# Kernel tuning notes

Measured on AMD Instinct MI355X. Metric: run time of the kernel, lower is better.

Reference implementation:

```python
import jax, jax.numpy as jnp
import numpy as np

EMBED_DIM = 1024
NUM_HEADS = 16
PROJ_DIM = EMBED_DIM // NUM_HEADS


def setup_inputs() -> dict:
    key = jax.random.key(0)
    ks = jax.random.split(key, 9)
    s = 1.0 / np.sqrt(EMBED_DIM)
    inp = {
        "inputs": jax.random.normal(ks[0], (4, 2048, EMBED_DIM), dtype=jnp.float32),
        "Wq": jax.random.normal(ks[1], (EMBED_DIM, EMBED_DIM), dtype=jnp.float32) * s,
        "bq": jnp.zeros((EMBED_DIM,), jnp.float32),
        "Wk": jax.random.normal(ks[2], (EMBED_DIM, EMBED_DIM), dtype=jnp.float32) * s,
        "bk": jnp.zeros((EMBED_DIM,), jnp.float32),
        "Wv": jax.random.normal(ks[3], (EMBED_DIM, EMBED_DIM), dtype=jnp.float32) * s,
        "bv": jnp.zeros((EMBED_DIM,), jnp.float32),
        "Wo": jax.random.normal(ks[4], (EMBED_DIM, EMBED_DIM), dtype=jnp.float32) * s,
        "bo": jnp.zeros((EMBED_DIM,), jnp.float32),
    }
    return inp


def _split_heads(x):
    # [B, S, E] -> [B, H, S, D]
    b, s, _ = x.shape
    return x.reshape(b, s, NUM_HEADS, PROJ_DIM).transpose(0, 2, 1, 3)


def reference(inputs, Wq, bq, Wk, bk, Wv, bv, Wo, bo):
    q = _split_heads(inputs @ Wq + bq)
    k = _split_heads(inputs @ Wk + bk)
    v = _split_heads(inputs @ Wv + bv)
    scale = 1.0 / jnp.sqrt(jnp.asarray(PROJ_DIM, inputs.dtype))
    scores = jnp.einsum("bhqd,bhkd->bhqk", q, k) * scale  # [B,H,S,S]
    weights = jax.nn.softmax(scores, axis=-1)
    attn = jnp.einsum("bhqk,bhkd->bhqd", weights, v)
    b, h, s, d = attn.shape
    concat = attn.transpose(0, 2, 1, 3).reshape(b, s, h * d)
    return concat @ Wo + bo
```

## Files before the change

kernel.cpp:

```cpp
#include <hip/hip_runtime.h>
#include <math.h>

#define EMB 1024
#define SEQ 2048
#define BATCH 4
#define NH 16
#define HD 64
#define MTOT (BATCH * SEQ)

typedef _Float16 half_t;
typedef _Float16 half8 __attribute__((ext_vector_type(8)));
typedef __fp16 fp16x2 __attribute__((ext_vector_type(2)));
typedef float floatx4 __attribute__((ext_vector_type(4)));
typedef float floatx16 __attribute__((ext_vector_type(16)));

#if __has_builtin(__builtin_amdgcn_exp2f)
#define EXP2(x) __builtin_amdgcn_exp2f(x)
#else
#define EXP2(x) exp2f(x)
#endif

#define QSCALE 0.18033688f

__device__ __forceinline__ unsigned pkh(float a, float b) {
  union { fp16x2 h; unsigned u; } c;
  c.h = __builtin_amdgcn_cvt_pkrtz(a, b);
  return c.u;
}

__global__ __launch_bounds__(256) void conv_all(const float* __restrict__ x,
                                                half_t* __restrict__ xh,
                                                const float* __restrict__ W0,
                                                const float* __restrict__ W1,
                                                const float* __restrict__ W2,
                                                const float* __restrict__ W3,
                                                half_t* __restrict__ wt) {
  __shared__ float T[64][68];
  const int bid = blockIdx.x;
  const int t = threadIdx.x;
  if (bid < 4096) {
    int i = bid * 256 + t;
    float4 a = ((const float4*)x)[i * 2];
    float4 b = ((const float4*)x)[i * 2 + 1];
    float v[8] = {a.x, a.y, a.z, a.w, b.x, b.y, b.z, b.w};
    half8 o;
#pragma unroll
    for (int j = 0; j < 8; ++j) o[j] = (half_t)v[j];
    *(half8*)(xh + (size_t)i * 8) = o;
    return;
  }
  const int b2 = bid - 4096;
  const int z = b2 >> 8, rem = b2 & 255;
  const int k0 = (rem >> 4) * 64, n0 = (rem & 15) * 64;
  const float* W = (z == 0) ? W0 : (z == 1) ? W1 : (z == 2) ? W2 : W3;
  half_t* wto = wt + (size_t)z * 1048576;
#pragma unroll
  for (int i = 0; i < 4; ++i) {
    int idx = t + i * 256;
    int row = idx >> 4, c4 = (idx & 15) << 2;
    *(float4*)(&T[row][c4]) = *(const float4*)(W + (size_t)(k0 + row) * EMB + n0 + c4);
  }
  __syncthreads();
#pragma unroll
  for (int cc = 0; cc < 2; ++cc) {
    int c = t + cc * 256;
    int n = c >> 3, g = c & 7;
    half8 hh;
#pragma unroll
    for (int j = 0; j < 8; ++j) hh[j] = (half_t)T[g * 8 + j][n];
    *(half8*)(wto + (size_t)(n0 + n) * EMB + k0 + g * 8) = hh;
  }
}

__global__ __launch_bounds__(256) void gemm_qkv(const half_t* __restrict__ A,
                                                const half_t* __restrict__ WT,
                                                const float* __restrict__ bq,
                                                const float* __restrict__ bk,
                                                const float* __restrict__ bvv,
                                                half_t* __restrict__ Qh,
                                                half_t* __restrict__ Kh,
                                                half_t* __restrict__ Vt) {
  __shared__ half_t lds[17408];
  half_t* As = lds;
  half_t* Bs = lds + 5120;

  const int mat = blockIdx.x;
  const half_t* B = WT + (size_t)mat * 1048576;
  const float* bias = (mat == 0) ? bq : (mat == 1) ? bk : bvv;
  const float scale = (mat == 0) ? QSCALE : 1.0f;
  half_t* outh = (mat == 0) ? Qh : (mat == 1) ? Kh : Vt;

  const int t = threadIdx.x;
  const int l = t & 63, w = t >> 6;
  const int wm = w >> 1, wn = w & 1;
  const int lr = l & 15, lg = l >> 4;
  const int row0 = blockIdx.y * 128, col0 = blockIdx.z * 128;
  const int sr = t >> 2, sg = t & 3;

  floatx4 acc[4][4];
#pragma unroll
  for (int i = 0; i < 4; ++i)
#pragma unroll
    for (int j = 0; j < 4; ++j) acc[i][j] = (floatx4){0.f, 0.f, 0.f, 0.f};

  for (int kb = 0; kb < EMB; kb += 32) {
    half8 a0 = *(const half8*)(A + (size_t)(row0 + sr) * EMB + kb + sg * 8);
    half8 a1 = *(const half8*)(A + (size_t)(row0 + sr + 64) * EMB + kb + sg * 8);
    half8 b0 = *(const half8*)(B + (size_t)(col0 + sr) * EMB + kb + sg * 8);
    half8 b1 = *(const half8*)(B + (size_t)(col0 + sr + 64) * EMB + kb + sg * 8);
    __syncthreads();
    *(half8*)(As + sr * 40 + sg * 8) = a0;
    *(half8*)(As + (sr + 64) * 40 + sg * 8) = a1;
    *(half8*)(Bs + sr * 40 + sg * 8) = b0;
    *(half8*)(Bs + (sr + 64) * 40 + sg * 8) = b1;
    __syncthreads();

    half8 fa[4];
#pragma unroll
    for (int mf = 0; mf < 4; ++mf)
      fa[mf] = *(const half8*)(As + (wm * 64 + mf * 16 + lr) * 40 + lg * 8);
#pragma unroll
    for (int nf = 0; nf < 4; ++nf) {
      half8 fb = *(const half8*)(Bs + (wn * 64 + nf * 16 + lr) * 40 + lg * 8);
#pragma unroll
      for (int mf = 0; mf < 4; ++mf)
        acc[mf][nf] = __builtin_amdgcn_mfma_f32_16x16x32_f16(fa[mf], fb, acc[mf][nf], 0, 0, 0);
    }
  }

  float bv[4];
#pragma unroll
  for (int nf = 0; nf < 4; ++nf) bv[nf] = bias[col0 + wn * 64 + nf * 16 + lr];

  if (mat < 2) {
#pragma unroll
    for (int mf = 0; mf < 4; ++mf)
#pragma unroll
      for (int nf = 0; nf < 4; ++nf)
#pragma unroll
        for (int r = 0; r < 4; ++r) {
          int row = row0 + wm * 64 + mf * 16 + lg * 4 + r;
          int col = col0 + wn * 64 + nf * 16 + lr;
          int bb = row >> 11, ss = row & (SEQ - 1);
          int hh = col >> 6, dd = col & (HD - 1);
          float f = (acc[mf][nf][r] + bv[nf]) * scale;
          outh[((size_t)(bb * NH + hh) * SEQ + ss) * HD + dd] = (half_t)f;
        }
  } else {
    half_t* T = lds;
    const int bb = row0 >> 11, s0 = row0 & (SEQ - 1);
    __syncthreads();
#pragma unroll
    for (int mf = 0; mf < 4; ++mf)
#pragma unroll
      for (int nf = 0; nf < 4; ++nf)
#pragma unroll
        for (int r = 0; r < 4; ++r) {
          float f = acc[mf][nf][r] + bv[nf];
          T[(wm * 64 + mf * 16 + lg * 4 + r) * 136 + wn * 64 + nf * 16 + lr] = (half_t)f;
        }
    __syncthreads();
#pragma unroll
    for (int i = 0; i < 8; ++i) {
      int idx = t + i * 256;
      int n = idx >> 4, mg = idx & 15;
      int col = col0 + n;
      int hh = col >> 6, dd = col & (HD - 1);
      half8 pk;
#pragma unroll
      for (int j = 0; j < 8; ++j) pk[j] = T[(mg * 8 + j) * 136 + n];
      *(half8*)(outh + ((size_t)(bb * NH + hh) * HD + dd) * SEQ + s0 + mg * 8) = pk;
    }
  }
}

__global__ __launch_bounds__(256) void gemmo(const half_t* __restrict__ A,
                                             const half_t* __restrict__ B,
                                             const float* __restrict__ bias,
                                             float* __restrict__ outf) {
  __shared__ half_t lds[10240];
  half_t* As = lds;
  half_t* Bs = lds + 5120;

  const int t = threadIdx.x;
  const int l = t & 63, w = t >> 6;
  const int wm = w >> 1, wn = w & 1;
  const int lr = l & 15, lg = l >> 4;
  const int row0 = blockIdx.x * 128, col0 = blockIdx.y * 128;
  const int sr = t >> 2, sg = t & 3;

  floatx4 acc[4][4];
#pragma unroll
  for (int i = 0; i < 4; ++i)
#pragma unroll
    for (int j = 0; j < 4; ++j) acc[i][j] = (floatx4){0.f, 0.f, 0.f, 0.f};

  for (int kb = 0; kb < EMB; kb += 32) {
    half8 a0 = *(const half8*)(A + (size_t)(row0 + sr) * EMB + kb + sg * 8);
    half8 a1 = *(const half8*)(A + (size_t)(row0 + sr + 64) * EMB + kb + sg * 8);
    half8 b0 = *(const half8*)(B + (size_t)(col0 + sr) * EMB + kb + sg * 8);
    half8 b1 = *(const half8*)(B + (size_t)(col0 + sr + 64) * EMB + kb + sg * 8);
    __syncthreads();
    *(half8*)(As + sr * 40 + sg * 8) = a0;
    *(half8*)(As + (sr + 64) * 40 + sg * 8) = a1;
    *(half8*)(Bs + sr * 40 + sg * 8) = b0;
    *(half8*)(Bs + (sr + 64) * 40 + sg * 8) = b1;
    __syncthreads();

    half8 fa[4];
#pragma unroll
    for (int mf = 0; mf < 4; ++mf)
      fa[mf] = *(const half8*)(As + (wm * 64 + mf * 16 + lr) * 40 + lg * 8);
#pragma unroll
    for (int nf = 0; nf < 4; ++nf) {
      half8 fb = *(const half8*)(Bs + (wn * 64 + nf * 16 + lr) * 40 + lg * 8);
#pragma unroll
      for (int mf = 0; mf < 4; ++mf)
        acc[mf][nf] = __builtin_amdgcn_mfma_f32_16x16x32_f16(fa[mf], fb, acc[mf][nf], 0, 0, 0);
    }
  }

  float bv[4];
#pragma unroll
  for (int nf = 0; nf < 4; ++nf) bv[nf] = bias[col0 + wn * 64 + nf * 16 + lr];
#pragma unroll
  for (int mf = 0; mf < 4; ++mf)
#pragma unroll
    for (int nf = 0; nf < 4; ++nf)
#pragma unroll
      for (int r = 0; r < 4; ++r) {
        int row = row0 + wm * 64 + mf * 16 + lg * 4 + r;
        int col = col0 + wn * 64 + nf * 16 + lr;
        outf[(size_t)row * EMB + col] = acc[mf][nf][r] + bv[nf];
      }
}

__global__ __launch_bounds__(512) void attnh(const half_t* __restrict__ Q,
                                             const half_t* __restrict__ K,
                                             const half_t* __restrict__ Vt,
                                             half_t* __restrict__ att) {
  __shared__ half_t lds[2 * 4608];
  half_t* Ks = lds;
  half_t* Vs = lds + 4608;

  const int t = threadIdx.x, l = t & 63, wq = t >> 6;
  const int lq = l & 31, hi = l >> 5;
  const int hi8 = hi * 8, hi4 = hi * 4;
  const int q0 = blockIdx.x * 256;
  const int bh = blockIdx.y;
  const size_t kbase = (size_t)bh * SEQ * HD;
  const size_t vbase = (size_t)bh * HD * SEQ;
  const int srow = t >> 3, sg = t & 7;

  half8 qf[4];
  const int qrow = q0 + wq * 32 + lq;
#pragma unroll
  for (int s = 0; s < 4; ++s)
    qf[s] = *(const half8*)(Q + kbase + (size_t)qrow * HD + s * 16 + hi8);

  floatx16 o0, o1;
#pragma unroll
  for (int r = 0; r < 16; ++r) { o0[r] = 0.f; o1[r] = 0.f; }
  float l_s = 0.f;

  half8 kh_r = *(const half8*)(K + kbase + (size_t)srow * HD + sg * 8);
  half8 vh_r = *(const half8*)(Vt + vbase + (size_t)srow * SEQ + sg * 8);

  for (int kv = 0; kv < SEQ; kv += 64) {
    __syncthreads();
    *(half8*)(Ks + srow * 72 + sg * 8) = kh_r;
    *(half8*)(Vs + srow * 72 + sg * 8) = vh_r;
    __syncthreads();

    {
      int nk = (kv + 64) & (SEQ - 1);
      kh_r = *(const half8*)(K + kbase + (size_t)(nk + srow) * HD + sg * 8);
      vh_r = *(const half8*)(Vt + vbase + (size_t)srow * SEQ + nk + sg * 8);
    }

    floatx16 s0v, s1v;
#pragma unroll
    for (int r = 0; r < 16; ++r) { s0v[r] = 0.f; s1v[r] = 0.f; }
#pragma unroll
    for (int s = 0; s < 4; ++s) {
      const int off = s * 16 + hi8;
      half8 kf0 = *(const half8*)(Ks + lq * 72 + off);
      half8 kf1 = *(const half8*)(Ks + (32 + lq) * 72 + off);
      s0v = __builtin_amdgcn_mfma_f32_32x32x16_f16(kf0, qf[s], s0v, 0, 0, 0);
      s1v = __builtin_amdgcn_mfma_f32_32x32x16_f16(kf1, qf[s], s1v, 0, 0, 0);
    }

    float rsum = 0.f;
#pragma unroll
    for (int r = 0; r < 16; ++r) { s0v[r] = EXP2(s0v[r]); rsum += s0v[r]; }
#pragma unroll
    for (int r = 0; r < 16; ++r) { s1v[r] = EXP2(s1v[r]); rsum += s1v[r]; }
    rsum += __shfl_xor(rsum, 32);
    l_s += rsum;

#define PV_STEP(SC, RH, S)                                                    \
  {                                                                           \
    unsigned u0 = pkh(SC[(RH) * 8 + 0], SC[(RH) * 8 + 1]);                    \
    unsigned u1 = pkh(SC[(RH) * 8 + 2], SC[(RH) * 8 + 3]);                    \
    unsigned u2 = pkh(SC[(RH) * 8 + 4], SC[(RH) * 8 + 5]);                    \
    unsigned u3 = pkh(SC[(RH) * 8 + 6], SC[(RH) * 8 + 7]);                    \
    asm volatile("v_permlane32_swap_b32 %0, %1" : "+v"(u0), "+v"(u2));        \
    asm volatile("v_permlane32_swap_b32 %0, %1" : "+v"(u1), "+v"(u3));        \
    int4 pi = make_int4((int)u0, (int)u1, (int)u2, (int)u3);                  \
    half8 pa = *(half8*)&pi;                                                  \
    half8 vb0 = *(const half8*)(Vs + lq * 72 + (S) * 16 + hi8);               \
    half8 vb1 = *(const half8*)(Vs + (32 + lq) * 72 + (S) * 16 + hi8);        \
    o0 = __builtin_amdgcn_mfma_f32_32x32x16_f16(pa, vb0, o0, 0, 0, 0);        \
    o1 = __builtin_amdgcn_mfma_f32_32x32x16_f16(pa, vb1, o1, 0, 0, 0);        \
  }
    PV_STEP(s0v, 0, 0)
    PV_STEP(s0v, 1, 1)
    PV_STEP(s1v, 0, 2)
    PV_STEP(s1v, 1, 3)
#undef PV_STEP
  }

  float inv = 1.f / l_s;
  float il[16];
#pragma unroll
  for (int r = 0; r < 16; ++r)
    il[r] = __shfl(inv, ((r & 3) + 8 * (r >> 2)) + hi4);
  const int bb2 = bh >> 4, hh2 = bh & 15;
#pragma unroll
  for (int dblk = 0; dblk < 2; ++dblk)
#pragma unroll
    for (int r = 0; r < 16; ++r) {
      float f = (dblk ? o1[r] : o0[r]) * il[r];
      int qg = q0 + wq * 32 + ((r & 3) + 8 * (r >> 2)) + hi4;
      size_t off = ((size_t)bb2 * SEQ + qg) * EMB + hh2 * HD + dblk * 32 + lq;
      att[off] = (half_t)f;
    }
}

extern "C" void kernel_launch(void* const* d_in, const int* in_sizes, int n_in,
                              void* d_out, int out_size, void* d_ws, size_t ws_size,
                              hipStream_t stream) {
  const float* X  = (const float*)d_in[0];
  const float* Wq = (const float*)d_in[1];
  const float* bq = (const float*)d_in[2];
  const float* Wk = (const float*)d_in[3];
  const float* bk = (const float*)d_in[4];
  const float* Wv = (const float*)d_in[5];
  const float* bv = (const float*)d_in[6];
  const float* Wo = (const float*)d_in[7];
  const float* bo = (const float*)d_in[8];
  float* out = (float*)d_out;

  char* wsb = (char*)d_ws;
  const size_t MB = 1024 * 1024;
  half_t* Xh = (half_t*)(wsb);
  half_t* WT = (half_t*)(wsb + 17 * MB);
  half_t* Qh = (half_t*)(wsb + 26 * MB);
  half_t* Kh = (half_t*)(wsb + 43 * MB);
  half_t* Vt = (half_t*)d_out;
  half_t* att = Xh;

  half_t* WTq = WT;
  half_t* WTo = WT + 3145728;

  conv_all<<<dim3(5120), 256, 0, stream>>>(X, Xh, Wq, Wk, Wv, Wo, WT);

  gemm_qkv<<<dim3(3, MTOT / 128, EMB / 128), 256, 0, stream>>>(
      Xh, WTq, bq, bk, bv, Qh, Kh, Vt);

  attnh<<<dim3(SEQ / 256, BATCH * NH), 512, 0, stream>>>(Qh, Kh, Vt, att);

  gemmo<<<dim3(MTOT / 128, EMB / 128), 256, 0, stream>>>(att, WTo, bo, out);
}
```

Baseline: 223.8 us.

## Load GEMM tiles directly into LDS with XOR-swizzled unpadded layout

Both projection GEMMs now use global_load_lds (16-byte direct global-to-LDS loads) instead of loading into registers and storing to shared memory. The padded 40-half row stride becomes an unpadded 32-half stride with an XOR swizzle on the 8-half chunk index to avoid bank conflicts on fragment reads. The V transpose staging buffer stride also changes from 136 to 137. This removes the register round-trip and shrinks LDS use, but keeps single buffering with two barriers per k-step, so load latency is still not overlapped.

Result: faster. 196.9 us (-12.0%).

```diff
diff --git a/kernel.cpp b/kernel.cpp
--- a/kernel.cpp
+++ b/kernel.cpp
@@ -21,6 +21,11 @@
 #endif
 
 #define QSCALE 0.18033688f
+
+#define GLOAD16(gsrc, ldst)                                                   \
+  __builtin_amdgcn_global_load_lds(                                           \
+      (__attribute__((address_space(1))) void*)(gsrc),                        \
+      (__attribute__((address_space(3))) void*)(ldst), 16, 0, 0)
 
 __device__ __forceinline__ unsigned pkh(float a, float b) {
   union { fp16x2 h; unsigned u; } c;
@@ -80,9 +85,9 @@
                                                 half_t* __restrict__ Qh,
                                                 half_t* __restrict__ Kh,
                                                 half_t* __restrict__ Vt) {
-  __shared__ half_t lds[17408];
+  __shared__ half_t lds[17536];
   half_t* As = lds;
-  half_t* Bs = lds + 5120;
+  half_t* Bs = lds + 4096;
 
   const int mat = blockIdx.x;
   const half_t* B = WT + (size_t)mat * 1048576;
@@ -95,7 +100,10 @@
   const int wm = w >> 1, wn = w & 1;
   const int lr = l & 15, lg = l >> 4;
   const int row0 = blockIdx.y * 128, col0 = blockIdx.z * 128;
-  const int sr = t >> 2, sg = t & 3;
+
+  const int sr2 = (w << 4) + (l >> 2);
+  const int swz = (l & 3) ^ (sr2 & 3);
+  const int rdsw = (lg ^ (lr & 3)) << 3;
 
   floatx4 acc[4][4];
 #pragma unroll
@@ -104,24 +112,22 @@
     for (int j = 0; j < 4; ++j) acc[i][j] = (floatx4){0.f, 0.f, 0.f, 0.f};
 
   for (int kb = 0; kb < EMB; kb += 32) {
-    half8 a0 = *(const half8*)(A + (size_t)(row0 + sr) * EMB + kb + sg * 8);
-    half8 a1 = *(const half8*)(A + (size_t)(row0 + sr + 64) * EMB + kb + sg * 8);
-    half8 b0 = *(const half8*)(B + (size_t)(col0 + sr) * EMB + kb + sg * 8);
-    half8 b1 = *(const half8*)(B + (size_t)(col0 + sr + 64) * EMB + kb + sg * 8);
-    __syncthreads();
-    *(half8*)(As + sr * 40 + sg * 8) = a0;
-    *(half8*)(As + (sr + 64) * 40 + sg * 8) = a1;
-    *(half8*)(Bs + sr * 40 + sg * 8) = b0;
-    *(half8*)(Bs + (sr + 64) * 40 + sg * 8) = b1;
+    __syncthreads();
+    GLOAD16(A + (size_t)(row0 + sr2) * EMB + kb + swz * 8, As + ((w << 4) << 5));
+    GLOAD16(A + (size_t)(row0 + 64 + sr2) * EMB + kb + swz * 8,
+            As + ((64 + (w << 4)) << 5));
+    GLOAD16(B + (size_t)(col0 + sr2) * EMB + kb + swz * 8, Bs + ((w << 4) << 5));
+    GLOAD16(B + (size_t)(col0 + 64 + sr2) * EMB + kb + swz * 8,
+            Bs + ((64 + (w << 4)) << 5));
     __syncthreads();
 
     half8 fa[4];
 #pragma unroll
     for (int mf = 0; mf < 4; ++mf)
-      fa[mf] = *(const half8*)(As + (wm * 64 + mf * 16 + lr) * 40 + lg * 8);
+      fa[mf] = *(const half8*)(As + ((wm * 64 + mf * 16 + lr) << 5) + rdsw);
 #pragma unroll
     for (int nf = 0; nf < 4; ++nf) {
-      half8 fb = *(const half8*)(Bs + (wn * 64 + nf * 16 + lr) * 40 + lg * 8);
+      half8 fb = *(const half8*)(Bs + ((wn * 64 + nf * 16 + lr) << 5) + rdsw);
 #pragma unroll
       for (int mf = 0; mf < 4; ++mf)
         acc[mf][nf] = __builtin_amdgcn_mfma_f32_16x16x32_f16(fa[mf], fb, acc[mf][nf], 0, 0, 0);
@@ -157,7 +163,7 @@
 #pragma unroll
         for (int r = 0; r < 4; ++r) {
           float f = acc[mf][nf][r] + bv[nf];
-          T[(wm * 64 + mf * 16 + lg * 4 + r) * 136 + wn * 64 + nf * 16 + lr] = (half_t)f;
+          T[(wm * 64 + mf * 16 + lg * 4 + r) * 137 + wn * 64 + nf * 16 + lr] = (half_t)f;
         }
     __syncthreads();
 #pragma unroll
@@ -168,7 +174,7 @@
       int hh = col >> 6, dd = col & (HD - 1);
       half8 pk;
 #pragma unroll
-      for (int j = 0; j < 8; ++j) pk[j] = T[(mg * 8 + j) * 136 + n];
+      for (int j = 0; j < 8; ++j) pk[j] = T[(mg * 8 + j) * 137 + n];
       *(half8*)(outh + ((size_t)(bb * NH + hh) * HD + dd) * SEQ + s0 + mg * 8) = pk;
     }
   }
@@ -178,16 +184,18 @@
                                              const half_t* __restrict__ B,
                                              const float* __restrict__ bias,
                                              float* __restrict__ outf) {
-  __shared__ half_t lds[10240];
+  __shared__ half_t lds[8192];
   half_t* As = lds;
-  half_t* Bs = lds + 5120;
+  half_t* Bs = lds + 4096;
 
   const int t = threadIdx.x;
   const int l = t & 63, w = t >> 6;
   const int wm = w >> 1, wn = w & 1;
   const int lr = l & 15, lg = l >> 4;
   const int row0 = blockIdx.x * 128, col0 = blockIdx.y * 128;
-  const int sr = t >> 2, sg = t & 3;
+  const int sr2 = (w << 4) + (l >> 2);
+  const int swz = (l & 3) ^ (sr2 & 3);
+  const int rdsw = (lg ^ (lr & 3)) << 3;
 
   floatx4 acc[4][4];
 #pragma unroll
@@ -196,24 +204,22 @@
     for (int j = 0; j < 4; ++j) acc[i][j] = (floatx4){0.f, 0.f, 0.f, 0.f};
 
   for (int kb = 0; kb < EMB; kb += 32) {
-    half8 a0 = *(const half8*)(A + (size_t)(row0 + sr) * EMB + kb + sg * 8);
-    half8 a1 = *(const half8*)(A + (size_t)(row0 + sr + 64) * EMB + kb + sg * 8);
-    half8 b0 = *(const half8*)(B + (size_t)(col0 + sr) * EMB + kb + sg * 8);
-    half8 b1 = *(const half8*)(B + (size_t)(col0 + sr + 64) * EMB + kb + sg * 8);
-    __syncthreads();
-    *(half8*)(As + sr * 40 + sg * 8) = a0;
-    *(half8*)(As + (sr + 64) * 40 + sg * 8) = a1;
-    *(half8*)(Bs + sr * 40 + sg * 8) = b0;
-    *(half8*)(Bs + (sr + 64) * 40 + sg * 8) = b1;
+    __syncthreads();
+    GLOAD16(A + (size_t)(row0 + sr2) * EMB + kb + swz * 8, As + ((w << 4) << 5));
+    GLOAD16(A + (size_t)(row0 + 64 + sr2) * EMB + kb + swz * 8,
+            As + ((64 + (w << 4)) << 5));
+    GLOAD16(B + (size_t)(col0 + sr2) * EMB + kb + swz * 8, Bs + ((w << 4) << 5));
+    GLOAD16(B + (size_t)(col0 + 64 + sr2) * EMB + kb + swz * 8,
+            Bs + ((64 + (w << 4)) << 5));
     __syncthreads();
 
     half8 fa[4];
 #pragma unroll
     for (int mf = 0; mf < 4; ++mf)
-      fa[mf] = *(const half8*)(As + (wm * 64 + mf * 16 + lr) * 40 + lg * 8);
+      fa[mf] = *(const half8*)(As + ((wm * 64 + mf * 16 + lr) << 5) + rdsw);
 #pragma unroll
     for (int nf = 0; nf < 4; ++nf) {
-      half8 fb = *(const half8*)(Bs + (wn * 64 + nf * 16 + lr) * 40 + lg * 8);
+      half8 fb = *(const half8*)(Bs + ((wn * 64 + nf * 16 + lr) << 5) + rdsw);
 #pragma unroll
       for (int mf = 0; mf < 4; ++mf)
         acc[mf][nf] = __builtin_amdgcn_mfma_f32_16x16x32_f16(fa[mf], fb, acc[mf][nf], 0, 0, 0);
```
